# Kernel tuning notes

Hardware: AMD Instinct MI355X
Metric: run time of the kernel (lower is better)

Reference implementation:

```python
import jax, jax.numpy as jnp
import numpy as np

V, E, H = 32000, 256, 512  # vocab, embedding_size, hidden_size
B, T = 64, 512             # batch, seq_len


def setup_inputs() -> dict:
    key = jax.random.key(0)
    ks = jax.random.split(key, 8)
    inputs = jax.random.randint(ks[0], (B, T), 0, V)
    lengths = jax.random.randint(ks[1], (B,), 0, T)
    reset_indices = jax.random.randint(ks[2], (B, T), 0, 2, dtype=jnp.int32)
    # nn.Embedding: N(0,1) init with padding_idx row zeroed
    emb = jax.random.normal(ks[3], (V, E), dtype=jnp.float32).at[0].set(0.0)
    # nn.LSTMCell params: uniform(-1/sqrt(H), 1/sqrt(H)), gate order i,f,g,o
    s = 1.0 / np.sqrt(H)
    W_ih = jax.random.uniform(ks[4], (4 * H, E), minval=-s, maxval=s, dtype=jnp.float32)
    W_hh = jax.random.uniform(ks[5], (4 * H, H), minval=-s, maxval=s, dtype=jnp.float32)
    b_ih = jax.random.uniform(ks[6], (4 * H,), minval=-s, maxval=s, dtype=jnp.float32)
    b_hh = jax.random.uniform(ks[7], (4 * H,), minval=-s, maxval=s, dtype=jnp.float32)
    return {"inputs": inputs, "lengths": lengths, "reset_indices": reset_indices,
            "emb": emb, "W_ih": W_ih, "W_hh": W_hh, "b_ih": b_ih, "b_hh": b_hh}


def reference(inputs, lengths, reset_indices, emb, W_ih, W_hh, b_ih, b_hh):
    x = emb[inputs]                                        # (B,T,E); dropout is identity in eval
    mask = (jnp.arange(T) < lengths[:, None]).astype(x.dtype)   # (B,T) length mask
    xt = jnp.swapaxes(x, 0, 1)                             # (T,B,E) time-major
    m_t = mask.T                                           # (T,B)
    r_t = reset_indices.astype(x.dtype).T                  # (T,B)
    # precompute input contribution to gates for all timesteps
    gates_x = jnp.einsum('tbe,ge->tbg', xt, W_ih) + b_ih + b_hh  # (T,B,4H)

    def step(carry, inp):
        h, c = carry
        gx, m, r = inp
        g = gx + h @ W_hh.T                                # (B,4H)
        i, f, gg, o = jnp.split(g, 4, axis=-1)
        i = jax.nn.sigmoid(i); f = jax.nn.sigmoid(f)
        gg = jnp.tanh(gg); o = jax.nn.sigmoid(o)
        c_new = f * c + i * gg
        h_new = o * jnp.tanh(c_new)
        mm = m[:, None]; rr = r[:, None]
        h_next = h_new * mm + h * (1 - mm)                 # mask-blend (keep state past length)
        c_next = c_new * mm + c * (1 - mm)
        # reset zeroing applied to carried state AFTER output is recorded
        return (h_next * (1 - rr), c_next * (1 - rr)), h_next

    h0 = jnp.zeros((B, H), dtype=x.dtype)
    (hT, cT), out_t = jax.lax.scan(step, (h0, h0), (gates_x, m_t, r_t))  # out_t: (T,B,H)
    output = jnp.swapaxes(out_t, 0, 1)                     # (B,T,H) = output.transpose(0,1)
    return output, hT, cT, mask
```

## Files before the change

kernel.cpp:

```cpp
#include <hip/hip_runtime.h>
#include <stdint.h>
#include <stddef.h>

constexpr int V = 32000, E = 256, H = 512, B = 64, T = 512;
constexpr int NTHR = 512;
constexpr int NBLK = 128;
constexpr int BATG = 16;
constexpr int HPB = 32;

constexpr int PSW = 128 * 17;
constexpr int OFF_PS   = 0;
constexpr int OFF_BIAS = OFF_PS + 8 * PSW * 4;
constexpr int OFF_LEN  = OFF_BIAS + 128 * 4;
constexpr int LDS_BYTES = 84 * 1024;

constexpr size_t OUT_HT   = (size_t)B * T * H;
constexpr size_t OUT_CT   = OUT_HT + (size_t)B * H;
constexpr size_t OUT_MASK = OUT_CT + (size_t)B * H;

typedef __attribute__((ext_vector_type(8))) short short8;
typedef __attribute__((ext_vector_type(4))) float f32x4;
typedef __attribute__((ext_vector_type(4))) unsigned int u32x4;

__device__ __forceinline__ unsigned short f2bf(float f) {
  uint32_t u = __builtin_bit_cast(uint32_t, f);
  return (unsigned short)((u + 0x7fffu + ((u >> 16) & 1u)) >> 16);
}
__device__ __forceinline__ short8 pack_bf8(float4 v0, float4 v1) {
  short8 r;
  r[0] = (short)f2bf(v0.x); r[1] = (short)f2bf(v0.y);
  r[2] = (short)f2bf(v0.z); r[3] = (short)f2bf(v0.w);
  r[4] = (short)f2bf(v1.x); r[5] = (short)f2bf(v1.y);
  r[6] = (short)f2bf(v1.z); r[7] = (short)f2bf(v1.w);
  return r;
}
__device__ __forceinline__ float sigmoidf_fast(float x) {
  return 1.f / (1.f + __expf(-x));
}
__device__ __forceinline__ float tanhf_fast(float x) {
  return 1.f - 2.f / (__expf(2.f * x) + 1.f);
}
__device__ __forceinline__ void st_h_dual(uint32_t* pl2, uint32_t* pml,
                                          uint32_t v) {
  asm volatile(
      "global_store_dword %0, %2, off\n\t"
      "global_store_dword %1, %2, off sc1"
      :: "v"(pl2), "v"(pml), "v"(v)
      : "memory");
}
__device__ __forceinline__ void ld_l2_k64(const uint32_t* p, u32x4& r0,
                                          u32x4& r1, u32x4& r2, u32x4& r3) {
  asm volatile(
      "global_load_dwordx4 %0, %4, off sc0\n\t"
      "global_load_dwordx4 %1, %4, off offset:16 sc0\n\t"
      "global_load_dwordx4 %2, %4, off offset:128 sc0\n\t"
      "global_load_dwordx4 %3, %4, off offset:144 sc0\n\t"
      "s_waitcnt vmcnt(0)"
      : "=&v"(r0), "=&v"(r1), "=&v"(r2), "=&v"(r3)
      : "v"(p)
      : "memory");
}
__device__ __forceinline__ void ld_mall_k64(const uint32_t* p, u32x4& r0,
                                            u32x4& r1, u32x4& r2, u32x4& r3) {
  asm volatile(
      "global_load_dwordx4 %0, %4, off sc1\n\t"
      "global_load_dwordx4 %1, %4, off offset:16 sc1\n\t"
      "global_load_dwordx4 %2, %4, off offset:128 sc1\n\t"
      "global_load_dwordx4 %3, %4, off offset:144 sc1\n\t"
      "s_waitcnt vmcnt(0)"
      : "=&v"(r0), "=&v"(r1), "=&v"(r2), "=&v"(r3)
      : "v"(p)
      : "memory");
}
__device__ __forceinline__ short8 cvt_frag(u32x4 lo, u32x4 hi) {
  uint32_t d0, d1, d2, d3;
  asm("v_cvt_pk_bf16_f32 %0, %1, %2" : "=v"(d0) : "v"(lo[0]), "v"(lo[1]));
  asm("v_cvt_pk_bf16_f32 %0, %1, %2" : "=v"(d1) : "v"(lo[2]), "v"(lo[3]));
  asm("v_cvt_pk_bf16_f32 %0, %1, %2" : "=v"(d2) : "v"(hi[0]), "v"(hi[1]));
  asm("v_cvt_pk_bf16_f32 %0, %1, %2" : "=v"(d3) : "v"(hi[2]), "v"(hi[3]));
  u32x4 d = {d0, d1, d2, d3};
  return __builtin_bit_cast(short8, d);
}

__global__ void __launch_bounds__(NTHR, 1)
lstm_mfma(const int* __restrict__ inputs, const int* __restrict__ lengths,
          const int* __restrict__ resets, const float* __restrict__ emb,
          const float* __restrict__ W_ih, const float* __restrict__ W_hh,
          const float* __restrict__ b_ih, const float* __restrict__ b_hh,
          float* __restrict__ out, uint32_t* __restrict__ hL2,
          uint32_t* __restrict__ hML) {
  extern __shared__ char lds[];
  float* Ps = (float*)(lds + OFF_PS);
  float* Bias = (float*)(lds + OFF_BIAS);
  int* Lens = (int*)(lds + OFF_LEN);

  const int tid = threadIdx.x;
  const int blk = blockIdx.x;
  const int grp = blk & 7;
  if (grp >= 4) return;
  const int rq = blk >> 3;
  const int vblk = grp * 16 + rq;
  const int khid = rq * HPB;
  const int b0 = grp * BATG;

  const int w = tid >> 6;
  const int L = tid & 63;
  const int lc = L & 15;
  const int q = L >> 4;

  short8 wfh[2][8];
  short8 wfe[8];
  #pragma unroll
  for (int s = 0; s < 2; ++s) {
    #pragma unroll
    for (int tl = 0; tl < 8; ++tl) {
      const int n = 16 * tl + lc;
      const int grow = (n >> 5) * H + khid + (n & 31);
      const float* src = W_hh + (size_t)grow * H + 64 * w + 32 * s + 8 * q;
      wfh[s][tl] = pack_bf8(*(const float4*)src, *(const float4*)(src + 4));
    }
  }
  #pragma unroll
  for (int tl = 0; tl < 8; ++tl) {
    const int n = 16 * tl + lc;
    const int grow = (n >> 5) * H + khid + (n & 31);
    const float* src = W_ih + (size_t)grow * E + 32 * w + 8 * q;
    wfe[tl] = pack_bf8(*(const float4*)src, *(const float4*)(src + 4));
  }
  if (tid < 128) {
    const int grow = (tid >> 5) * H + khid + (tid & 31);
    Bias[tid] = b_ih[grow] + b_hh[grow];
  }
  if (tid < 16) Lens[tid] = lengths[b0 + tid];
  {
    int i = vblk * 512 + tid;
    int mb = i >> 9, mt = i & (T - 1);
    out[OUT_MASK + i] = (mt < lengths[mb]) ? 1.f : 0.f;
  }
  __syncthreads();

  const int jj = tid & 31;
  const int bb = tid >> 5;

  float carry_h = 0.f, carry_c = 0.f;
  bool fb = false;

  for (int t = 0; t < T; ++t) {
    const size_t srcbase = (size_t)(t & 1) * (B * H);
    const size_t dstbase = (size_t)((t + 1) & 1) * (B * H);

    float rr = (float)resets[(b0 + bb) * T + t];
    const int tok = inputs[(b0 + lc) * T + t];
    const float* eb = emb + (size_t)tok * E + 32 * w + 8 * q;
    short8 ae = pack_bf8(*(const float4*)eb, *(const float4*)(eb + 4));
    f32x4 acc[8];
    const f32x4 zero4 = {0.f, 0.f, 0.f, 0.f};
    #pragma unroll
    for (int tl = 0; tl < 8; ++tl)
      acc[tl] = __builtin_amdgcn_mfma_f32_16x16x32_bf16(ae, wfe[tl], zero4, 0, 0, 0);

    if (t > 0) {
      const uint32_t expect = 4u | (((uint32_t)(t - 1) >> 1) & 3u);
      const size_t off = srcbase + (size_t)(b0 + lc) * H + 64 * w + 8 * q;
      const uint32_t* pl2 = hL2 + off;
      const uint32_t* pml = hML + off;
      u32x4 r0, r1, r2, r3;
      int spins = 0;
      for (;;) {
        if (!fb) ld_l2_k64(pl2, r0, r1, r2, r3);
        else     ld_mall_k64(pml, r0, r1, r2, r3);
        uint32_t o = (r0[0] | r0[1] | r0[2] | r0[3]) |
                     (r1[0] | r1[1] | r1[2] | r1[3]) |
                     (r2[0] | r2[1] | r2[2] | r2[3]) |
                     (r3[0] | r3[1] | r3[2] | r3[3]);
        uint32_t a = (r0[0] & r0[1] & r0[2] & r0[3]) &
                     (r1[0] & r1[1] & r1[2] & r1[3]) &
                     (r2[0] & r2[1] & r2[2] & r2[3]) &
                     (r3[0] & r3[1] & r3[2] & r3[3]);
        uint32_t bad = ((o ^ expect) | (a ^ expect)) & 7u;
        if (!__any((int)bad)) break;
        if (!fb && ++spins >= 64) fb = true;
      }
      short8 a0 = cvt_frag(r0, r1);
      short8 a1 = cvt_frag(r2, r3);
      #pragma unroll
      for (int tl = 0; tl < 8; ++tl)
        acc[tl] = __builtin_amdgcn_mfma_f32_16x16x32_bf16(a0, wfh[0][tl], acc[tl], 0, 0, 0);
      #pragma unroll
      for (int tl = 0; tl < 8; ++tl)
        acc[tl] = __builtin_amdgcn_mfma_f32_16x16x32_bf16(a1, wfh[1][tl], acc[tl], 0, 0, 0);
    }

    #pragma unroll
    for (int tl = 0; tl < 8; ++tl)
      *(f32x4*)(Ps + w * PSW + (16 * tl + lc) * 17 + 4 * q) = acc[tl];
    __syncthreads();

    float g4[4];
    #pragma unroll
    for (int gi = 0; gi < 4; ++gi) {
      const int n = gi * 32 + jj;
      float s = Bias[n];
      #pragma unroll
      for (int ww = 0; ww < 8; ++ww) s += Ps[ww * PSW + n * 17 + bb];
      g4[gi] = s;
    }
    __syncthreads();

    float ig = sigmoidf_fast(g4[0]);
    float fg = sigmoidf_fast(g4[1]);
    float gg = tanhf_fast(g4[2]);
    float og = sigmoidf_fast(g4[3]);
    float c_new = fg * carry_c + ig * gg;
    float h_new = og * tanhf_fast(c_new);
    bool live = (t < Lens[bb]);
    float h_next = live ? h_new : carry_h;
    float c_next = live ? c_new : carry_c;
    carry_h = h_next * (1.f - rr);
    carry_c = c_next * (1.f - rr);

    if (t < T - 1) {
      const uint32_t wtag = 4u | (((uint32_t)t >> 1) & 3u);
      uint32_t bits = (__builtin_bit_cast(uint32_t, carry_h) & ~7u) | wtag;
      const size_t doff = dstbase + (size_t)(b0 + bb) * H + HPB * rq + jj;
      st_h_dual(hL2 + doff, hML + doff, bits);
    }
    out[((size_t)(b0 + bb) * T + t) * H + khid + jj] = h_next;
  }
  out[OUT_HT + (size_t)(b0 + bb) * H + khid + jj] = carry_h;
  out[OUT_CT + (size_t)(b0 + bb) * H + khid + jj] = carry_c;
}

extern "C" void kernel_launch(void* const* d_in, const int* in_sizes, int n_in,
                              void* d_out, int out_size, void* d_ws, size_t ws_size,
                              hipStream_t stream) {
  const int* inputs    = (const int*)d_in[0];
  const int* lengths   = (const int*)d_in[1];
  const int* resets    = (const int*)d_in[2];
  const float* emb     = (const float*)d_in[3];
  const float* W_ih    = (const float*)d_in[4];
  const float* W_hh    = (const float*)d_in[5];
  const float* b_ih    = (const float*)d_in[6];
  const float* b_hh    = (const float*)d_in[7];
  float* out = (float*)d_out;

  constexpr size_t HBYTES = (size_t)2 * B * H * 4;
  uint32_t* hL2 = (uint32_t*)d_ws;
  uint32_t* hML = (uint32_t*)((char*)d_ws + HBYTES);

  hipFuncSetAttribute((const void*)lstm_mfma,
                      hipFuncAttributeMaxDynamicSharedMemorySize, LDS_BYTES);

  hipMemsetAsync(d_ws, 0, 2 * HBYTES, stream);
  lstm_mfma<<<NBLK, NTHR, LDS_BYTES, stream>>>(
      inputs, lengths, resets, emb, W_ih, W_hh, b_ih, b_hh, out, hL2, hML);
}
```

Baseline: 2.110 ms.

## Interleave gate rows so each thread reduces its four gates with vector LDS reads

After: 2.542 ms. +20.5%, slower.

```diff
diff --git a/kernel.cpp b/kernel.cpp
--- a/kernel.cpp
+++ b/kernel.cpp
@@ -8,9 +8,9 @@
 constexpr int BATG = 16;
 constexpr int HPB = 32;
 
-constexpr int PSW = 128 * 17;
-constexpr int OFF_PS   = 0;
-constexpr int OFF_BIAS = OFF_PS + 8 * PSW * 4;
+constexpr int PGW = 2048;
+constexpr int OFF_PG   = 0;
+constexpr int OFF_BIAS = OFF_PG + 8 * PGW * 4;
 constexpr int OFF_LEN  = OFF_BIAS + 128 * 4;
 constexpr int LDS_BYTES = 84 * 1024;
 
@@ -39,6 +39,9 @@
 }
 __device__ __forceinline__ float tanhf_fast(float x) {
   return 1.f - 2.f / (__expf(2.f * x) + 1.f);
+}
+__device__ __forceinline__ void bar_lgkm() {
+  asm volatile("s_waitcnt lgkmcnt(0)\n\ts_barrier" ::: "memory");
 }
 __device__ __forceinline__ void st_h_dual(uint32_t* pl2, uint32_t* pml,
                                           uint32_t v) {
@@ -90,7 +93,7 @@
           float* __restrict__ out, uint32_t* __restrict__ hL2,
           uint32_t* __restrict__ hML) {
   extern __shared__ char lds[];
-  float* Ps = (float*)(lds + OFF_PS);
+  float* Pg = (float*)(lds + OFF_PG);
   float* Bias = (float*)(lds + OFF_BIAS);
   int* Lens = (int*)(lds + OFF_LEN);
 
@@ -114,22 +117,22 @@
   for (int s = 0; s < 2; ++s) {
     #pragma unroll
     for (int tl = 0; tl < 8; ++tl) {
-      const int n = 16 * tl + lc;
-      const int grow = (n >> 5) * H + khid + (n & 31);
+      const int p = 16 * tl + lc;
+      const int grow = (p & 3) * H + khid + (p >> 2);
       const float* src = W_hh + (size_t)grow * H + 64 * w + 32 * s + 8 * q;
       wfh[s][tl] = pack_bf8(*(const float4*)src, *(const float4*)(src + 4));
     }
   }
   #pragma unroll
   for (int tl = 0; tl < 8; ++tl) {
-    const int n = 16 * tl + lc;
-    const int grow = (n >> 5) * H + khid + (n & 31);
+    const int p = 16 * tl + lc;
+    const int grow = (p & 3) * H + khid + (p >> 2);
     const float* src = W_ih + (size_t)grow * E + 32 * w + 8 * q;
     wfe[tl] = pack_bf8(*(const float4*)src, *(const float4*)(src + 4));
   }
   if (tid < 128) {
-    const int grow = (tid >> 5) * H + khid + (tid & 31);
-    Bias[tid] = b_ih[grow] + b_hh[grow];
+    const int g = tid & 3, jl = tid >> 2;
+    Bias[tid] = b_ih[g * H + khid + jl] + b_hh[g * H + khid + jl];
   }
   if (tid < 16) Lens[tid] = lengths[b0 + tid];
   {
@@ -139,25 +142,31 @@
   }
   __syncthreads();
 
-  const int jj = tid & 31;
-  const int bb = tid >> 5;
-
+  const int jloc = 4 * w + q;
   float carry_h = 0.f, carry_c = 0.f;
   bool fb = false;
+
+  float rr_cur = (float)resets[(b0 + lc) * T + 0];
+  const float* eb0 = emb + (size_t)inputs[(b0 + lc) * T + 0] * E + 32 * w + 8 * q;
+  float4 e0 = *(const float4*)eb0, e1 = *(const float4*)(eb0 + 4);
 
   for (int t = 0; t < T; ++t) {
     const size_t srcbase = (size_t)(t & 1) * (B * H);
     const size_t dstbase = (size_t)((t + 1) & 1) * (B * H);
 
-    float rr = (float)resets[(b0 + bb) * T + t];
-    const int tok = inputs[(b0 + lc) * T + t];
-    const float* eb = emb + (size_t)tok * E + 32 * w + 8 * q;
-    short8 ae = pack_bf8(*(const float4*)eb, *(const float4*)(eb + 4));
+    short8 ae = pack_bf8(e0, e1);
+    const float rr = rr_cur;
+    int tok_n = 0; float rr_n = 0.f;
+    if (t < T - 1) {
+      tok_n = inputs[(b0 + lc) * T + t + 1];
+      rr_n = (float)resets[(b0 + lc) * T + t + 1];
+    }
+
     f32x4 acc[8];
     const f32x4 zero4 = {0.f, 0.f, 0.f, 0.f};
     #pragma unroll
     for (int tl = 0; tl < 8; ++tl)
-      acc[tl] = __builtin_amdgcn_mfma_f32_16x16x32_bf16(ae, wfe[tl], zero4, 0, 0, 0);
+      acc[tl] = __builtin_amdgcn_mfma_f32_16x16x32_bf16(wfe[tl], ae, zero4, 0, 0, 0);
 
     if (t > 0) {
       const uint32_t expect = 4u | (((uint32_t)(t - 1) >> 1) & 3u);
@@ -185,27 +194,29 @@
       short8 a1 = cvt_frag(r2, r3);
       #pragma unroll
       for (int tl = 0; tl < 8; ++tl)
-        acc[tl] = __builtin_amdgcn_mfma_f32_16x16x32_bf16(a0, wfh[0][tl], acc[tl], 0, 0, 0);
+        acc[tl] = __builtin_amdgcn_mfma_f32_16x16x32_bf16(wfh[0][tl], a0, acc[tl], 0, 0, 0);
       #pragma unroll
       for (int tl = 0; tl < 8; ++tl)
-        acc[tl] = __builtin_amdgcn_mfma_f32_16x16x32_bf16(a1, wfh[1][tl], acc[tl], 0, 0, 0);
+        acc[tl] = __builtin_amdgcn_mfma_f32_16x16x32_bf16(wfh[1][tl], a1, acc[tl], 0, 0, 0);
+    }
+
+    if (t < T - 1) {
+      const float* ebn = emb + (size_t)tok_n * E + 32 * w + 8 * q;
+      e0 = *(const float4*)ebn;
+      e1 = *(const float4*)(ebn + 4);
+      rr_cur = rr_n;
     }
 
     #pragma unroll
     for (int tl = 0; tl < 8; ++tl)
-      *(f32x4*)(Ps + w * PSW + (16 * tl + lc) * 17 + 4 * q) = acc[tl];
-    __syncthreads();
-
-    float g4[4];
-    #pragma unroll
-    for (int gi = 0; gi < 4; ++gi) {
-      const int n = gi * 32 + jj;
-      float s = Bias[n];
-      #pragma unroll
-      for (int ww = 0; ww < 8; ++ww) s += Ps[ww * PSW + n * 17 + bb];
-      g4[gi] = s;
-    }
-    __syncthreads();
+      *(f32x4*)(Pg + w * PGW + (4 * tl + q) * 64 + lc * 4) = acc[tl];
+    bar_lgkm();
+
+    f32x4 g4 = *(const f32x4*)(Bias + jloc * 4);
+    #pragma unroll
+    for (int ww = 0; ww < 8; ++ww)
+      g4 += *(const f32x4*)(Pg + ww * PGW + jloc * 64 + lc * 4);
+    bar_lgkm();
 
     float ig = sigmoidf_fast(g4[0]);
     float fg = sigmoidf_fast(g4[1]);
@@ -213,7 +224,7 @@
     float og = sigmoidf_fast(g4[3]);
     float c_new = fg * carry_c + ig * gg;
     float h_new = og * tanhf_fast(c_new);
-    bool live = (t < Lens[bb]);
+    bool live = (t < Lens[lc]);
     float h_next = live ? h_new : carry_h;
     float c_next = live ? c_new : carry_c;
     carry_h = h_next * (1.f - rr);
@@ -222,13 +233,13 @@
     if (t < T - 1) {
       const uint32_t wtag = 4u | (((uint32_t)t >> 1) & 3u);
       uint32_t bits = (__builtin_bit_cast(uint32_t, carry_h) & ~7u) | wtag;
-      const size_t doff = dstbase + (size_t)(b0 + bb) * H + HPB * rq + jj;
+      const size_t doff = dstbase + (size_t)(b0 + lc) * H + khid + jloc;
       st_h_dual(hL2 + doff, hML + doff, bits);
     }
-    out[((size_t)(b0 + bb) * T + t) * H + khid + jj] = h_next;
-  }
-  out[OUT_HT + (size_t)(b0 + bb) * H + khid + jj] = carry_h;
-  out[OUT_CT + (size_t)(b0 + bb) * H + khid + jj] = carry_c;
+    out[((size_t)(b0 + lc) * T + t) * H + khid + jloc] = h_next;
+  }
+  out[OUT_HT + (size_t)(b0 + lc) * H + khid + jloc] = carry_h;
+  out[OUT_CT + (size_t)(b0 + lc) * H + khid + jloc] = carry_c;
 }
 
 extern "C" void kernel_launch(void* const* d_in, const int* in_sizes, int n_in,
```

## Prefetch next-step embeddings, batch output stores via LDS, and add spinning filler blocks

Applied to the files above, without the earlier changes.

After: 1.967 ms. -6.8%, faster.

```diff
diff --git a/kernel.cpp b/kernel.cpp
--- a/kernel.cpp
+++ b/kernel.cpp
@@ -12,7 +12,8 @@
 constexpr int OFF_PS   = 0;
 constexpr int OFF_BIAS = OFF_PS + 8 * PSW * 4;
 constexpr int OFF_LEN  = OFF_BIAS + 128 * 4;
-constexpr int LDS_BYTES = 84 * 1024;
+constexpr int OFF_OBUF = 70400;
+constexpr int LDS_BYTES = 88 * 1024;
 
 constexpr size_t OUT_HT   = (size_t)B * T * H;
 constexpr size_t OUT_CT   = OUT_HT + (size_t)B * H;
@@ -39,6 +40,9 @@
 }
 __device__ __forceinline__ float tanhf_fast(float x) {
   return 1.f - 2.f / (__expf(2.f * x) + 1.f);
+}
+__device__ __forceinline__ void bar_lgkm() {
+  asm volatile("s_waitcnt lgkmcnt(0)\n\ts_barrier" ::: "memory");
 }
 __device__ __forceinline__ void st_h_dual(uint32_t* pl2, uint32_t* pml,
                                           uint32_t v) {
@@ -88,16 +92,30 @@
           const float* __restrict__ W_ih, const float* __restrict__ W_hh,
           const float* __restrict__ b_ih, const float* __restrict__ b_hh,
           float* __restrict__ out, uint32_t* __restrict__ hL2,
-          uint32_t* __restrict__ hML) {
+          uint32_t* __restrict__ hML, uint32_t* __restrict__ done) {
+  const int tid = threadIdx.x;
+  const int blk = blockIdx.x;
+  const int grp = blk & 7;
+  if (grp >= 4) {
+    float x = 1.0000001f;
+    const float y = 0.99990f + 1e-7f * (float)blk;
+    for (;;) {
+      #pragma unroll 64
+      for (int i = 0; i < 512; ++i) x = __builtin_fmaf(x, y, 1e-4f);
+      asm volatile("" :: "v"(x));
+      uint32_t d = __hip_atomic_load(done, __ATOMIC_RELAXED,
+                                     __HIP_MEMORY_SCOPE_AGENT);
+      if (d >= 64u) break;
+    }
+    return;
+  }
+
   extern __shared__ char lds[];
   float* Ps = (float*)(lds + OFF_PS);
   float* Bias = (float*)(lds + OFF_BIAS);
   int* Lens = (int*)(lds + OFF_LEN);
-
-  const int tid = threadIdx.x;
-  const int blk = blockIdx.x;
-  const int grp = blk & 7;
-  if (grp >= 4) return;
+  float* Obuf = (float*)(lds + OFF_OBUF);
+
   const int rq = blk >> 3;
   const int vblk = grp * 16 + rq;
   const int khid = rq * HPB;
@@ -145,90 +163,119 @@
   float carry_h = 0.f, carry_c = 0.f;
   bool fb = false;
 
-  for (int t = 0; t < T; ++t) {
-    const size_t srcbase = (size_t)(t & 1) * (B * H);
-    const size_t dstbase = (size_t)((t + 1) & 1) * (B * H);
-
-    float rr = (float)resets[(b0 + bb) * T + t];
-    const int tok = inputs[(b0 + lc) * T + t];
-    const float* eb = emb + (size_t)tok * E + 32 * w + 8 * q;
-    short8 ae = pack_bf8(*(const float4*)eb, *(const float4*)(eb + 4));
-    f32x4 acc[8];
-    const f32x4 zero4 = {0.f, 0.f, 0.f, 0.f};
-    #pragma unroll
-    for (int tl = 0; tl < 8; ++tl)
-      acc[tl] = __builtin_amdgcn_mfma_f32_16x16x32_bf16(ae, wfe[tl], zero4, 0, 0, 0);
-
-    if (t > 0) {
-      const uint32_t expect = 4u | (((uint32_t)(t - 1) >> 1) & 3u);
-      const size_t off = srcbase + (size_t)(b0 + lc) * H + 64 * w + 8 * q;
-      const uint32_t* pl2 = hL2 + off;
-      const uint32_t* pml = hML + off;
-      u32x4 r0, r1, r2, r3;
-      int spins = 0;
-      for (;;) {
-        if (!fb) ld_l2_k64(pl2, r0, r1, r2, r3);
-        else     ld_mall_k64(pml, r0, r1, r2, r3);
-        uint32_t o = (r0[0] | r0[1] | r0[2] | r0[3]) |
-                     (r1[0] | r1[1] | r1[2] | r1[3]) |
-                     (r2[0] | r2[1] | r2[2] | r2[3]) |
-                     (r3[0] | r3[1] | r3[2] | r3[3]);
-        uint32_t a = (r0[0] & r0[1] & r0[2] & r0[3]) &
-                     (r1[0] & r1[1] & r1[2] & r1[3]) &
-                     (r2[0] & r2[1] & r2[2] & r2[3]) &
-                     (r3[0] & r3[1] & r3[2] & r3[3]);
-        uint32_t bad = ((o ^ expect) | (a ^ expect)) & 7u;
-        if (!__any((int)bad)) break;
-        if (!fb && ++spins >= 64) fb = true;
-      }
-      short8 a0 = cvt_frag(r0, r1);
-      short8 a1 = cvt_frag(r2, r3);
+  float rr_cur = (float)resets[(b0 + bb) * T + 0];
+  const float* eb0 =
+      emb + (size_t)inputs[(b0 + lc) * T + 0] * E + 32 * w + 8 * q;
+  float4 e0 = *(const float4*)eb0, e1 = *(const float4*)(eb0 + 4);
+
+  for (int tb = 0; tb < T / 8; ++tb) {
+    #pragma unroll 1
+    for (int ts = 0; ts < 8; ++ts) {
+      const int t = tb * 8 + ts;
+      const size_t srcbase = (size_t)(t & 1) * (B * H);
+      const size_t dstbase = (size_t)((t + 1) & 1) * (B * H);
+
+      short8 ae = pack_bf8(e0, e1);
+      const float rr = rr_cur;
+      int tok_n = 0; float rr_n = 0.f;
+      if (t < T - 1) {
+        tok_n = inputs[(b0 + lc) * T + t + 1];
+        rr_n = (float)resets[(b0 + bb) * T + t + 1];
+      }
+
+      f32x4 acc[8];
+      const f32x4 zero4 = {0.f, 0.f, 0.f, 0.f};
       #pragma unroll
       for (int tl = 0; tl < 8; ++tl)
-        acc[tl] = __builtin_amdgcn_mfma_f32_16x16x32_bf16(a0, wfh[0][tl], acc[tl], 0, 0, 0);
+        acc[tl] = __builtin_amdgcn_mfma_f32_16x16x32_bf16(ae, wfe[tl], zero4, 0, 0, 0);
+
+      if (t > 0) {
+        const uint32_t expect = 4u | (((uint32_t)(t - 1) >> 1) & 3u);
+        const size_t off = srcbase + (size_t)(b0 + lc) * H + 64 * w + 8 * q;
+        const uint32_t* pl2 = hL2 + off;
+        const uint32_t* pml = hML + off;
+        u32x4 r0, r1, r2, r3;
+        int spins = 0;
+        for (;;) {
+          if (!fb) ld_l2_k64(pl2, r0, r1, r2, r3);
+          else     ld_mall_k64(pml, r0, r1, r2, r3);
+          uint32_t o = (r0[0] | r0[1] | r0[2] | r0[3]) |
+                       (r1[0] | r1[1] | r1[2] | r1[3]) |
+                       (r2[0] | r2[1] | r2[2] | r2[3]) |
+                       (r3[0] | r3[1] | r3[2] | r3[3]);
+          uint32_t a = (r0[0] & r0[1] & r0[2] & r0[3]) &
+                       (r1[0] & r1[1] & r1[2] & r1[3]) &
+                       (r2[0] & r2[1] & r2[2] & r2[3]) &
+                       (r3[0] & r3[1] & r3[2] & r3[3]);
+          uint32_t bad = ((o ^ expect) | (a ^ expect)) & 7u;
+          if (!__any((int)bad)) break;
+          if (!fb && ++spins >= 64) fb = true;
+        }
+        short8 a0 = cvt_frag(r0, r1);
+        short8 a1 = cvt_frag(r2, r3);
+        #pragma unroll
+        for (int tl = 0; tl < 8; ++tl)
+          acc[tl] = __builtin_amdgcn_mfma_f32_16x16x32_bf16(a0, wfh[0][tl], acc[tl], 0, 0, 0);
+        #pragma unroll
+        for (int tl = 0; tl < 8; ++tl)
+          acc[tl] = __builtin_amdgcn_mfma_f32_16x16x32_bf16(a1, wfh[1][tl], acc[tl], 0, 0, 0);
+      }
+
+      if (t < T - 1) {
+        const float* ebn = emb + (size_t)tok_n * E + 32 * w + 8 * q;
+        e0 = *(const float4*)ebn;
+        e1 = *(const float4*)(ebn + 4);
+        rr_cur = rr_n;
+      }
+
       #pragma unroll
       for (int tl = 0; tl < 8; ++tl)
-        acc[tl] = __builtin_amdgcn_mfma_f32_16x16x32_bf16(a1, wfh[1][tl], acc[tl], 0, 0, 0);
+        *(f32x4*)(Ps + w * PSW + (16 * tl + lc) * 17 + 4 * q) = acc[tl];
+      bar_lgkm();
+
+      float g4[4];
+      #pragma unroll
+      for (int gi = 0; gi < 4; ++gi) {
+        const int n = gi * 32 + jj;
+        float s = Bias[n];
+        #pragma unroll
+        for (int ww = 0; ww < 8; ++ww) s += Ps[ww * PSW + n * 17 + bb];
+        g4[gi] = s;
+      }
+      bar_lgkm();
+
+      float ig = sigmoidf_fast(g4[0]);
+      float fg = sigmoidf_fast(g4[1]);
+      float gg = tanhf_fast(g4[2]);
+      float og = sigmoidf_fast(g4[3]);
+      float c_new = fg * carry_c + ig * gg;
+      float h_new = og * tanhf_fast(c_new);
+      bool live = (t < Lens[bb]);
+      float h_next = live ? h_new : carry_h;
+      float c_next = live ? c_new : carry_c;
+      carry_h = h_next * (1.f - rr);
+      carry_c = c_next * (1.f - rr);
+
+      if (t < T - 1) {
+        const uint32_t wtag = 4u | (((uint32_t)t >> 1) & 3u);
+        uint32_t bits = (__builtin_bit_cast(uint32_t, carry_h) & ~7u) | wtag;
+        const size_t doff = dstbase + (size_t)(b0 + bb) * H + khid + jj;
+        st_h_dual(hL2 + doff, hML + doff, bits);
+      }
+      Obuf[ts * 512 + tid] = h_next;
     }
-
     #pragma unroll
-    for (int tl = 0; tl < 8; ++tl)
-      *(f32x4*)(Ps + w * PSW + (16 * tl + lc) * 17 + 4 * q) = acc[tl];
-    __syncthreads();
-
-    float g4[4];
-    #pragma unroll
-    for (int gi = 0; gi < 4; ++gi) {
-      const int n = gi * 32 + jj;
-      float s = Bias[n];
-      #pragma unroll
-      for (int ww = 0; ww < 8; ++ww) s += Ps[ww * PSW + n * 17 + bb];
-      g4[gi] = s;
-    }
-    __syncthreads();
-
-    float ig = sigmoidf_fast(g4[0]);
-    float fg = sigmoidf_fast(g4[1]);
-    float gg = tanhf_fast(g4[2]);
-    float og = sigmoidf_fast(g4[3]);
-    float c_new = fg * carry_c + ig * gg;
-    float h_new = og * tanhf_fast(c_new);
-    bool live = (t < Lens[bb]);
-    float h_next = live ? h_new : carry_h;
-    float c_next = live ? c_new : carry_c;
-    carry_h = h_next * (1.f - rr);
-    carry_c = c_next * (1.f - rr);
-
-    if (t < T - 1) {
-      const uint32_t wtag = 4u | (((uint32_t)t >> 1) & 3u);
-      uint32_t bits = (__builtin_bit_cast(uint32_t, carry_h) & ~7u) | wtag;
-      const size_t doff = dstbase + (size_t)(b0 + bb) * H + HPB * rq + jj;
-      st_h_dual(hL2 + doff, hML + doff, bits);
-    }
-    out[((size_t)(b0 + bb) * T + t) * H + khid + jj] = h_next;
+    for (int ts = 0; ts < 8; ++ts)
+      out[((size_t)(b0 + bb) * T + (tb * 8 + ts)) * H + khid + jj] =
+          Obuf[ts * 512 + tid];
   }
   out[OUT_HT + (size_t)(b0 + bb) * H + khid + jj] = carry_h;
   out[OUT_CT + (size_t)(b0 + bb) * H + khid + jj] = carry_c;
+  asm volatile("s_waitcnt vmcnt(0)" ::: "memory");
+  __syncthreads();
+  if (tid == 0)
+    __hip_atomic_fetch_add(done, 1u, __ATOMIC_RELAXED,
+                           __HIP_MEMORY_SCOPE_AGENT);
 }
 
 extern "C" void kernel_launch(void* const* d_in, const int* in_sizes, int n_in,
@@ -245,13 +292,15 @@
   float* out = (float*)d_out;
 
   constexpr size_t HBYTES = (size_t)2 * B * H * 4;
-  uint32_t* hL2 = (uint32_t*)d_ws;
-  uint32_t* hML = (uint32_t*)((char*)d_ws + HBYTES);
+  uint32_t* hL2  = (uint32_t*)d_ws;
+  uint32_t* hML  = (uint32_t*)((char*)d_ws + HBYTES);
+  uint32_t* done = (uint32_t*)((char*)d_ws + 2 * HBYTES);
 
   hipFuncSetAttribute((const void*)lstm_mfma,
                       hipFuncAttributeMaxDynamicSharedMemorySize, LDS_BYTES);
 
-  hipMemsetAsync(d_ws, 0, 2 * HBYTES, stream);
+  hipMemsetAsync(d_ws, 0, 2 * HBYTES + 4096, stream);
   lstm_mfma<<<NBLK, NTHR, LDS_BYTES, stream>>>(
-      inputs, lengths, resets, emb, W_ih, W_hh, b_ih, b_hh, out, hL2, hML);
-}
+      inputs, lengths, resets, emb, W_ih, W_hh, b_ih, b_hh, out, hL2, hML,
+      done);
+}
```
